# Kernel tuning notes

Measured on AMD Instinct MI355X. Metric: run time of the kernel, lower is better.

The kernel has to match this reference:

```python
import jax, jax.numpy as jnp
import numpy as np

B, S, DMODEL = 1, 2048, 4096
H, HKV, DH = 32, 8, 128
LTAB, RBKT = 20, 128
NEG = -1e9


def rotate_half(x):
    x1, x2 = x[..., : x.shape[-1] // 2], x[..., x.shape[-1] // 2:]
    return jnp.concatenate((-x2, x1), axis=-1)


def setup_inputs() -> dict:
    key = jax.random.key(0)
    ks = jax.random.split(key, 12)
    inp = {
        "hidden_states": jax.random.normal(ks[0], (B, S, DMODEL), jnp.float32),
        "cos": jax.random.uniform(ks[1], (B, S, DH), jnp.float32),
        "sin": jax.random.uniform(ks[2], (B, S, DH), jnp.float32),
        "q_probs": jax.random.uniform(ks[3], (B, H, LTAB, RBKT), jnp.float32),
        "v_norm": jax.random.uniform(ks[4], (B, H, S), jnp.float32),
        "allowed": jnp.ones((B, H, S), dtype=bool),
        "k_hard": jax.random.randint(ks[5], (B, H, LTAB, S), 0, RBKT, jnp.int32),
        "Wq": jax.random.normal(ks[6], (DMODEL, H * DH), jnp.float32) * 0.02,
        "Wk": jax.random.normal(ks[7], (DMODEL, HKV * DH), jnp.float32) * 0.02,
        "Wv": jax.random.normal(ks[8], (DMODEL, HKV * DH), jnp.float32) * 0.02,
        "Wo": jax.random.normal(ks[9], (H * DH, DMODEL), jnp.float32) * 0.02,
        "sink": 4,
        "window": 128,
        "M": 256,
    }
    return inp


def _sparse_key_mask(q_probs, v_norm, allowed, k_hard, sink, window, M):
    """Faithful jax version of build_sparse_list_decode, returned as a boolean
    allowed-key mask [B, H, T] (equivalent to scattering sparse_list)."""
    Bm, Hm, _, T = k_hard.shape
    # soft-hash collision score: sum over tables of q bucket prob at key's bucket,
    # weighted by value-norm history, restricted to allowed keys.
    coll = jnp.take_along_axis(q_probs, k_hard.astype(jnp.int32), axis=-1).sum(axis=2)  # [B,H,T]
    scores = jnp.where(allowed, coll * v_norm, -jnp.inf)
    M_eff = min(M, T)
    mask = jnp.zeros((Bm, Hm, T), dtype=bool)
    if M_eff > 0:
        heavy_idx = jax.lax.top_k(scores, M_eff)[1]  # [B,H,M]
        b_ix = jnp.arange(Bm)[:, None, None]
        h_ix = jnp.arange(Hm)[None, :, None]
        mask = mask.at[b_ix, h_ix, heavy_idx].set(True)
    sink = max(0, min(sink, T))
    window = max(0, min(window, T))
    if sink > 0:
        mask = mask.at[:, :, :sink].set(True)
    if window > 0:
        win_start = max(T - window, sink)
        if win_start < T:
            mask = mask.at[:, :, win_start:].set(True)
    if sink == 0 and window == 0:
        mask = mask.at[:, :, T - 1].set(True)
    return mask & allowed


def reference(hidden_states, cos, sin, q_probs, v_norm, allowed, k_hard,
              Wq, Wk, Wv, Wo, sink, window, M):
    Bx, Sx, _ = hidden_states.shape
    scaling = DH ** -0.5
    q = (hidden_states @ Wq).reshape(Bx, Sx, H, DH).transpose(0, 2, 1, 3)   # [B,H,S,Dh]
    k = (hidden_states @ Wk).reshape(Bx, Sx, HKV, DH).transpose(0, 2, 1, 3)  # [B,Hkv,S,Dh]
    v = (hidden_states @ Wv).reshape(Bx, Sx, HKV, DH).transpose(0, 2, 1, 3)
    # RoPE (unsqueeze_dim=1)
    c, s = cos[:, None, :, :], sin[:, None, :, :]
    q = q * c + rotate_half(q) * s
    k = k * c + rotate_half(k) * s
    # repeat_kv for GQA
    n_rep = H // HKV
    k = jnp.repeat(k, n_rep, axis=1)
    v = jnp.repeat(v, n_rep, axis=1)
    # sparse heavy-hitter + sink + window key mask (no_grad in the original)
    key_mask = _sparse_key_mask(q_probs, v_norm, allowed, k_hard, sink, window, M)  # [B,H,S]
    causal = jnp.tril(jnp.ones((Sx, Sx), dtype=bool))
    allow = causal[None, None] & key_mask[:, :, None, :]  # [B,H,S,S]
    scores = jnp.einsum('bhqd,bhkd->bhqk', q, k) * scaling
    attn = jax.nn.softmax(jnp.where(allow, scores, NEG), axis=-1)
    out = jnp.einsum('bhqk,bhkd->bhqd', attn, v)
    out = out.transpose(0, 2, 1, 3).reshape(Bx, Sx, H * DH)
    return out @ Wo
```

## Files before the change

kernel.cpp:

```cpp
#include <hip/hip_runtime.h>
#include <hip/hip_bf16.h>
#include <cstdint>
#include <cstddef>

namespace {

constexpr int S_LEN = 2048;
constexpr int DM    = 4096;
constexpr int NH    = 32;
constexpr int NKV   = 8;
constexpr int DH    = 128;
constexpr int LTAB  = 20;
constexpr int RBKT  = 128;
constexpr int NQKV  = NH * DH + 2 * NKV * DH;
constexpr int KOFF  = NH * DH;
constexpr int VOFF  = NH * DH + NKV * DH;

typedef short s16x8 __attribute__((ext_vector_type(8)));
typedef float f32x4 __attribute__((ext_vector_type(4)));
typedef unsigned long long u64;
struct u64x2 { u64 x, y; };

__device__ inline short bf16s(float f) {
  __hip_bfloat16 b = __float2bfloat16(f);
  return (short)*reinterpret_cast<unsigned short*>(&b);
}
__device__ inline float s2f(short s) {
  unsigned short u = (unsigned short)s;
  return __bfloat162float(*reinterpret_cast<__hip_bfloat16*>(&u));
}

__global__ __launch_bounds__(256) void cvt_f32_bf16(const float* __restrict__ in,
                                                    __hip_bfloat16* __restrict__ out,
                                                    int n4) {
  int i = blockIdx.x * blockDim.x + threadIdx.x;
  if (i >= n4) return;
  float4 v = reinterpret_cast<const float4*>(in)[i];
  ushort4 o;
  o.x = (unsigned short)bf16s(v.x);
  o.y = (unsigned short)bf16s(v.y);
  o.z = (unsigned short)bf16s(v.z);
  o.w = (unsigned short)bf16s(v.w);
  reinterpret_cast<ushort4*>(out)[i] = o;
}

__global__ __launch_bounds__(256) void transpose_cvt64(const float* __restrict__ W,
                                                       __hip_bfloat16* __restrict__ Wt,
                                                       int K, int N) {
  __shared__ float tile[64][65];
  const int kb = blockIdx.y * 64, nb = blockIdx.x * 64;
  const int tid = threadIdx.x;
  const int r0 = tid >> 4, c4 = (tid & 15) * 4;
#pragma unroll
  for (int it = 0; it < 4; ++it) {
    const int r = r0 + it * 16;
    float4 v = *reinterpret_cast<const float4*>(&W[(size_t)(kb + r) * N + nb + c4]);
    tile[r][c4] = v.x;
    tile[r][c4 + 1] = v.y;
    tile[r][c4 + 2] = v.z;
    tile[r][c4 + 3] = v.w;
  }
  __syncthreads();
  const int n0 = tid >> 4, k4 = (tid & 15) * 4;
#pragma unroll
  for (int it = 0; it < 4; ++it) {
    const int n = n0 + it * 16;
    ushort4 o;
    o.x = (unsigned short)bf16s(tile[k4][n]);
    o.y = (unsigned short)bf16s(tile[k4 + 1][n]);
    o.z = (unsigned short)bf16s(tile[k4 + 2][n]);
    o.w = (unsigned short)bf16s(tile[k4 + 3][n]);
    *reinterpret_cast<ushort4*>(&Wt[(size_t)(nb + n) * K + kb + k4]) = o;
  }
}

template <bool OUT_F32>
__global__ __launch_bounds__(256) void gemm_bt(const __hip_bfloat16* __restrict__ A,
                                               const __hip_bfloat16* __restrict__ Bt,
                                               void* __restrict__ Cout,
                                               int N, int K) {
  __shared__ __hip_bfloat16 As[128 * 64];
  __shared__ __hip_bfloat16 Bs[128 * 64];
  const int tid = threadIdx.x;
  const int wid = tid >> 6;
  const int lane = tid & 63;
  const int bm = blockIdx.y, bn = blockIdx.x;
  const int wr = wid >> 1, wc = wid & 1;
  f32x4 acc[4][4] = {};
  const __hip_bfloat16* Abase = A + (size_t)bm * 128 * K;
  const __hip_bfloat16* Bbase = Bt + (size_t)bn * 128 * K;
  for (int kt = 0; kt < K; kt += 64) {
    __syncthreads();
#pragma unroll
    for (int j = 0; j < 4; ++j) {
      const int pb = j * 4096 + wid * 1024;
      const int p = pb + lane * 16;
      const int row = p >> 7;
      const int slot = ((p >> 4) & 7) ^ (row & 7);
      const int goff = row * K + kt + slot * 8;
      __builtin_amdgcn_global_load_lds(
          (const __attribute__((address_space(1))) void*)(Abase + goff),
          (__attribute__((address_space(3))) void*)(As + (pb >> 1)), 16, 0, 0);
      __builtin_amdgcn_global_load_lds(
          (const __attribute__((address_space(1))) void*)(Bbase + goff),
          (__attribute__((address_space(3))) void*)(Bs + (pb >> 1)), 16, 0, 0);
    }
    __syncthreads();
#pragma unroll
    for (int kk = 0; kk < 2; ++kk) {
      s16x8 af[4], bf[4];
#pragma unroll
      for (int i = 0; i < 4; ++i) {
        const int ra = wr * 64 + i * 16 + (lane & 15);
        const int sa = (kk * 4 + (lane >> 4)) ^ (ra & 7);
        af[i] = *reinterpret_cast<const s16x8*>(As + ra * 64 + sa * 8);
        const int rb = wc * 64 + i * 16 + (lane & 15);
        const int sb = (kk * 4 + (lane >> 4)) ^ (rb & 7);
        bf[i] = *reinterpret_cast<const s16x8*>(Bs + rb * 64 + sb * 8);
      }
#pragma unroll
      for (int i = 0; i < 4; ++i)
#pragma unroll
        for (int jn = 0; jn < 4; ++jn)
          acc[i][jn] = __builtin_amdgcn_mfma_f32_16x16x32_bf16(af[i], bf[jn], acc[i][jn], 0, 0, 0);
    }
  }
  const int rg = (lane >> 4) * 4;
  const int cg = lane & 15;
#pragma unroll
  for (int i = 0; i < 4; ++i)
#pragma unroll
    for (int jn = 0; jn < 4; ++jn)
#pragma unroll
      for (int r = 0; r < 4; ++r) {
        const int rr = bm * 128 + wr * 64 + i * 16 + rg + r;
        const int cc = bn * 128 + wc * 64 + jn * 16 + cg;
        if (OUT_F32)
          reinterpret_cast<float*>(Cout)[(size_t)rr * N + cc] = acc[i][jn][r];
        else
          reinterpret_cast<__hip_bfloat16*>(Cout)[(size_t)rr * N + cc] =
              __float2bfloat16(acc[i][jn][r]);
      }
}

__global__ __launch_bounds__(256) void rope_kernel(const __hip_bfloat16* __restrict__ QKV,
                                                   const float* __restrict__ cosb,
                                                   const float* __restrict__ sinb,
                                                   __hip_bfloat16* __restrict__ Qro,
                                                   __hip_bfloat16* __restrict__ Kro) {
  const int s = blockIdx.x;
  const int tid = threadIdx.x;
  const float* cs = cosb + s * DH;
  const float* sn = sinb + s * DH;
  const __hip_bfloat16* row = QKV + (size_t)s * NQKV;
  for (int ch = tid; ch < 512 + 128; ch += 256) {
    const bool isQ = ch < 512;
    const int idx8 = (isQ ? ch : ch - 512) * 8;
    const int d8 = idx8 & (DH - 1);
    const int hb = idx8 - d8;
    const __hip_bfloat16* src = isQ ? row : row + KOFF;
    s16x8 v = *reinterpret_cast<const s16x8*>(src + idx8);
    s16x8 p = *reinterpret_cast<const s16x8*>(src + hb + (d8 ^ 64));
    const float sgn = (d8 < 64) ? -1.f : 1.f;
    s16x8 outv;
#pragma unroll
    for (int j = 0; j < 8; ++j) {
      const float r = s2f(v[j]) * cs[d8 + j] + sgn * s2f(p[j]) * sn[d8 + j];
      outv[j] = bf16s(r);
    }
    if (isQ)
      *reinterpret_cast<s16x8*>(Qro + (size_t)s * (NH * DH) + idx8) = outv;
    else
      *reinterpret_cast<s16x8*>(Kro + (size_t)s * (NKV * DH) + idx8) = outv;
  }
}

__global__ __launch_bounds__(1024) void select_kernel(const float* __restrict__ q_probs,
                                                      const float* __restrict__ v_norm,
                                                      const int* __restrict__ allowed,
                                                      const int* __restrict__ k_hard,
                                                      const int* __restrict__ sinkp,
                                                      const int* __restrict__ winp,
                                                      const int* __restrict__ Mp,
                                                      int* __restrict__ sel_idx,
                                                      int* __restrict__ sel_cnt) {
  const int h = blockIdx.x;
  const int tid = threadIdx.x;
  const int lane = tid & 63;
  const int wid = tid >> 6;
  __shared__ u64 keys[S_LEN];
  __shared__ int waveTot[16];
  const int t0 = tid * 2;
  float c0 = 0.f, c1 = 0.f;
#pragma unroll
  for (int l = 0; l < LTAB; ++l) {
    const int2 kh = *reinterpret_cast<const int2*>(&k_hard[(size_t)(h * LTAB + l) * S_LEN + t0]);
    c0 += q_probs[(h * LTAB + l) * RBKT + kh.x];
    c1 += q_probs[(h * LTAB + l) * RBKT + kh.y];
  }
  const int2 al = *reinterpret_cast<const int2*>(&allowed[h * S_LEN + t0]);
  const float2 vn = *reinterpret_cast<const float2*>(&v_norm[h * S_LEN + t0]);
  const float s0 = al.x ? c0 * vn.x : -INFINITY;
  const float s1 = al.y ? c1 * vn.y : -INFINITY;
  auto mkkey = [](float s, int t) -> u64 {
    unsigned m = __float_as_uint(s);
    m = (m & 0x80000000u) ? ~m : (m | 0x80000000u);
    return ((u64)m << 11) | (u64)(S_LEN - 1 - t);
  };
  const u64 k0 = mkkey(s0, t0);
  const u64 k1 = mkkey(s1, t0 + 1);
  keys[t0] = k0;
  keys[t0 + 1] = k1;
  __syncthreads();
  int r0 = 0, r1 = 0;
#pragma unroll 8
  for (int u = 0; u < S_LEN; u += 2) {
    const u64x2 kv = *reinterpret_cast<const u64x2*>(&keys[u]);
    r0 += (kv.x > k0) + (kv.y > k0);
    r1 += (kv.x > k1) + (kv.y > k1);
  }
  const int Mv = min(Mp[0], S_LEN);
  int sv = sinkp[0];
  sv = sv < 0 ? 0 : (sv > S_LEN ? S_LEN : sv);
  int wv = winp[0];
  wv = wv < 0 ? 0 : (wv > S_LEN ? S_LEN : wv);
  int wstart = S_LEN - wv;
  if (wstart < sv) wstart = sv;
  bool sel0 = r0 < Mv, sel1 = r1 < Mv;
  if (t0 < sv) sel0 = true;
  if (t0 + 1 < sv) sel1 = true;
  if (wv > 0) {
    if (t0 >= wstart) sel0 = true;
    if (t0 + 1 >= wstart) sel1 = true;
  }
  if (sv == 0 && wv == 0) {
    if (t0 == S_LEN - 1) sel0 = true;
    if (t0 + 1 == S_LEN - 1) sel1 = true;
  }
  sel0 = sel0 && (al.x != 0);
  sel1 = sel1 && (al.y != 0);
  const int cnt = (sel0 ? 1 : 0) + (sel1 ? 1 : 0);
  int inc = cnt;
#pragma unroll
  for (int off = 1; off < 64; off <<= 1) {
    int n = __shfl_up(inc, off);
    if (lane >= off) inc += n;
  }
  if (lane == 63) waveTot[wid] = inc;
  __syncthreads();
  int wbase = 0;
  for (int w = 0; w < wid; ++w) wbase += waveTot[w];
  int pos = wbase + inc - cnt;
  if (tid == 0) {
    int tot = 0;
#pragma unroll
    for (int w = 0; w < 16; ++w) tot += waveTot[w];
    sel_cnt[h] = tot;
  }
  if (sel0) sel_idx[h * S_LEN + pos++] = t0;
  if (sel1) sel_idx[h * S_LEN + pos] = t0 + 1;
}

__global__ __launch_bounds__(256) void attn_kernel(const __hip_bfloat16* __restrict__ Qro,
                                                   const __hip_bfloat16* __restrict__ Kro,
                                                   const __hip_bfloat16* __restrict__ Vpk,
                                                   const int* __restrict__ sel_idx,
                                                   const int* __restrict__ sel_cnt,
                                                   __hip_bfloat16* __restrict__ ctx) {
  constexpr int BKV = 32;
  const int h = blockIdx.y;
  const int q0 = blockIdx.x * 64;
  const int tid = threadIdx.x, wid = tid >> 6, lane = tid & 63;
  const int kv = h >> 2;
  __shared__ __hip_bfloat16 Ks[BKV][DH + 8];
  __shared__ __hip_bfloat16 Vt[DH][BKV + 8];
  __shared__ __hip_bfloat16 Ps[4][16][BKV + 8];
  __shared__ int tIdx[BKV];
  const int qbase = q0 + wid * 16;
  const float scaling = 0.08838834764831845f;
  s16x8 qf[4];
  {
    const __hip_bfloat16* qp =
        Qro + (size_t)(qbase + (lane & 15)) * (NH * DH) + h * DH + (lane >> 4) * 8;
#pragma unroll
    for (int kt = 0; kt < 4; ++kt) {
      s16x8 q = *reinterpret_cast<const s16x8*>(qp + kt * 32);
#pragma unroll
      for (int j = 0; j < 8; ++j) q[j] = bf16s(s2f(q[j]) * scaling);
      qf[kt] = q;
    }
  }
  float mr[4], lr[4];
#pragma unroll
  for (int r = 0; r < 4; ++r) {
    mr[r] = -3.0e38f;
    lr[r] = 0.f;
  }
  f32x4 o[8] = {};
  const int cnt = sel_cnt[h];
  const int qmax = q0 + 63;
  for (int j0 = 0; j0 < cnt; j0 += BKV) {
    if (sel_idx[h * S_LEN + j0] > qmax) break;
    const int nk = min(BKV, cnt - j0);
    __syncthreads();
    if (tid < BKV) tIdx[tid] = (tid < nk) ? sel_idx[h * S_LEN + j0 + tid] : 0x7fffffff;
#pragma unroll
    for (int c = 0; c < 2; ++c) {
      const int ch = tid + c * 256;
      const int row = ch >> 4, c8 = ch & 15;
      if (row < nk) {
        const int t = sel_idx[h * S_LEN + j0 + row];
        *reinterpret_cast<s16x8*>(&Ks[row][c8 * 8]) = *reinterpret_cast<const s16x8*>(
            Kro + (size_t)t * (NKV * DH) + kv * DH + c8 * 8);
      }
    }
    {
      const int j = tid >> 3;
      const int dp = (tid & 7) * 16;
      if (j < nk) {
        const int t = sel_idx[h * S_LEN + j0 + j];
        const __hip_bfloat16* vp = Vpk + (size_t)t * NQKV + kv * DH + dp;
        s16x8 a = *reinterpret_cast<const s16x8*>(vp);
        s16x8 b = *reinterpret_cast<const s16x8*>(vp + 8);
#pragma unroll
        for (int i = 0; i < 8; ++i) reinterpret_cast<short&>(Vt[dp + i][j]) = a[i];
#pragma unroll
        for (int i = 0; i < 8; ++i) reinterpret_cast<short&>(Vt[dp + 8 + i][j]) = b[i];
      } else {
#pragma unroll
        for (int i = 0; i < 16; ++i) reinterpret_cast<short&>(Vt[dp + i][j]) = 0;
      }
    }
    __syncthreads();
    f32x4 s0 = {0.f, 0.f, 0.f, 0.f}, s1 = {0.f, 0.f, 0.f, 0.f};
#pragma unroll
    for (int kt = 0; kt < 4; ++kt) {
      s16x8 k0 = *reinterpret_cast<const s16x8*>(&Ks[lane & 15][kt * 32 + (lane >> 4) * 8]);
      s16x8 k1 = *reinterpret_cast<const s16x8*>(&Ks[16 + (lane & 15)][kt * 32 + (lane >> 4) * 8]);
      s0 = __builtin_amdgcn_mfma_f32_16x16x32_bf16(qf[kt], k0, s0, 0, 0, 0);
      s1 = __builtin_amdgcn_mfma_f32_16x16x32_bf16(qf[kt], k1, s1, 0, 0, 0);
    }
    const int t0 = tIdx[lane & 15];
    const int t1 = tIdx[16 + (lane & 15)];
    float v0[4], v1[4], mx[4];
    bool need = false;
#pragma unroll
    for (int r = 0; r < 4; ++r) {
      const int qs = qbase + ((lane >> 4) << 2) + r;
      v0[r] = (t0 <= qs) ? s0[r] : -1.0e9f;
      v1[r] = (t1 <= qs) ? s1[r] : -1.0e9f;
      float m = fmaxf(v0[r], v1[r]);
#pragma unroll
      for (int off = 1; off < 16; off <<= 1) m = fmaxf(m, __shfl_xor(m, off));
      mx[r] = m;
      need = need || (m > mr[r] + 8.f);
    }
    if (__any(need)) {
#pragma unroll
      for (int r = 0; r < 4; ++r) {
        const float mn = fmaxf(mr[r], mx[r]);
        const float scl = __expf(mr[r] - mn);
        lr[r] *= scl;
#pragma unroll
        for (int nt = 0; nt < 8; ++nt) o[nt][r] *= scl;
        mr[r] = mn;
      }
    }
#pragma unroll
    for (int r = 0; r < 4; ++r) {
      const float p0 = __expf(v0[r] - mr[r]);
      const float p1 = __expf(v1[r] - mr[r]);
      float ps = p0 + p1;
#pragma unroll
      for (int off = 1; off < 16; off <<= 1) ps += __shfl_xor(ps, off);
      lr[r] += ps;
      Ps[wid][((lane >> 4) << 2) + r][lane & 15] = __float2bfloat16(p0);
      Ps[wid][((lane >> 4) << 2) + r][16 + (lane & 15)] = __float2bfloat16(p1);
    }
    const s16x8 pf = *reinterpret_cast<const s16x8*>(&Ps[wid][lane & 15][(lane >> 4) * 8]);
#pragma unroll
    for (int nt = 0; nt < 8; ++nt) {
      const s16x8 vf =
          *reinterpret_cast<const s16x8*>(&Vt[nt * 16 + (lane & 15)][(lane >> 4) * 8]);
      o[nt] = __builtin_amdgcn_mfma_f32_16x16x32_bf16(pf, vf, o[nt], 0, 0, 0);
    }
  }
#pragma unroll
  for (int nt = 0; nt < 8; ++nt)
#pragma unroll
    for (int r = 0; r < 4; ++r) {
      const int qs = qbase + ((lane >> 4) << 2) + r;
      const int d = nt * 16 + (lane & 15);
      ctx[(size_t)qs * (NH * DH) + h * DH + d] = __float2bfloat16(o[nt][r] / lr[r]);
    }
}

}

extern "C" void kernel_launch(void* const* d_in, const int* in_sizes, int n_in,
                              void* d_out, int out_size, void* d_ws, size_t ws_size,
                              hipStream_t stream) {
  const float* hidden = (const float*)d_in[0];
  const float* cosb = (const float*)d_in[1];
  const float* sinb = (const float*)d_in[2];
  const float* q_probs = (const float*)d_in[3];
  const float* v_norm = (const float*)d_in[4];
  const int* allowed = (const int*)d_in[5];
  const int* k_hard = (const int*)d_in[6];
  const float* Wq = (const float*)d_in[7];
  const float* Wk = (const float*)d_in[8];
  const float* Wv = (const float*)d_in[9];
  const float* Wo = (const float*)d_in[10];
  const int* sinkp = (const int*)d_in[11];
  const int* winp = (const int*)d_in[12];
  const int* Mp = (const int*)d_in[13];

  char* ws = (char*)d_ws;
  size_t off = 0;
  auto alloc = [&](size_t bytes) -> char* {
    char* p = ws + off;
    off += (bytes + 255) & ~(size_t)255;
    return p;
  };
  __hip_bfloat16* hbf = (__hip_bfloat16*)alloc((size_t)S_LEN * DM * 2);
  __hip_bfloat16* WqkvT = (__hip_bfloat16*)alloc((size_t)NQKV * DM * 2);
  __hip_bfloat16* WoT = (__hip_bfloat16*)alloc((size_t)DM * DM * 2);
  __hip_bfloat16* QKV = (__hip_bfloat16*)alloc((size_t)S_LEN * NQKV * 2);
  __hip_bfloat16* Qro = (__hip_bfloat16*)alloc((size_t)S_LEN * NH * DH * 2);
  __hip_bfloat16* Kro = (__hip_bfloat16*)alloc((size_t)S_LEN * NKV * DH * 2);
  __hip_bfloat16* ctx = (__hip_bfloat16*)alloc((size_t)S_LEN * NH * DH * 2);
  int* sel_idx = (int*)alloc((size_t)NH * S_LEN * 4);
  int* sel_cnt = (int*)alloc((size_t)NH * 4);
  if (off > ws_size) return;

  {
    const int n4 = S_LEN * DM / 4;
    cvt_f32_bf16<<<(n4 + 255) / 256, 256, 0, stream>>>(hidden, hbf, n4);
  }
  transpose_cvt64<<<dim3(DM / 64, DM / 64), 256, 0, stream>>>(Wq, WqkvT, DM, DM);
  transpose_cvt64<<<dim3((NKV * DH) / 64, DM / 64), 256, 0, stream>>>(
      Wk, WqkvT + (size_t)KOFF * DM, DM, NKV * DH);
  transpose_cvt64<<<dim3((NKV * DH) / 64, DM / 64), 256, 0, stream>>>(
      Wv, WqkvT + (size_t)VOFF * DM, DM, NKV * DH);
  transpose_cvt64<<<dim3(DM / 64, DM / 64), 256, 0, stream>>>(Wo, WoT, DM, DM);

  gemm_bt<false><<<dim3(NQKV / 128, S_LEN / 128), 256, 0, stream>>>(
      hbf, WqkvT, (void*)QKV, NQKV, DM);

  rope_kernel<<<S_LEN, 256, 0, stream>>>(QKV, cosb, sinb, Qro, Kro);

  select_kernel<<<NH, 1024, 0, stream>>>(q_probs, v_norm, allowed, k_hard, sinkp, winp, Mp,
                                         sel_idx, sel_cnt);

  attn_kernel<<<dim3(S_LEN / 64, NH), 256, 0, stream>>>(Qro, Kro, QKV + VOFF, sel_idx,
                                                        sel_cnt, ctx);

  gemm_bt<true><<<dim3(DM / 128, S_LEN / 128), 256, 0, stream>>>(ctx, WoT, d_out, DM, DM);
}
```

Measured before the change: 431.2 us.

## Swizzle GEMM block order and compute softmax row sums via MFMA

The GEMM remaps workgroup IDs so that consecutive blocks are interleaved across eight groups, aiming for better cache locality across XCDs. In the sparse attention kernel, the per-row max shuffle reduction now runs only when a rescale is triggered, using a per-lane threshold test. The row-sum shuffle reduction is replaced by an MFMA of the bf16 probabilities against a ones vector. The row sum therefore accumulates the bf16-rounded probabilities, which keeps it consistent with the PV product but changes numerics slightly.

```diff
diff --git a/kernel.cpp b/kernel.cpp
--- a/kernel.cpp
+++ b/kernel.cpp
@@ -84,7 +84,20 @@
   const int tid = threadIdx.x;
   const int wid = tid >> 6;
   const int lane = tid & 63;
-  const int bm = blockIdx.y, bn = blockIdx.x;
+  int bm, bn;
+  {
+    const int nwg = gridDim.x * gridDim.y;
+    const int orig = blockIdx.y * gridDim.x + blockIdx.x;
+    if ((nwg & 7) == 0) {
+      const int cpx = nwg >> 3;
+      const int id2 = (orig & 7) * cpx + (orig >> 3);
+      bm = id2 / gridDim.x;
+      bn = id2 % gridDim.x;
+    } else {
+      bm = blockIdx.y;
+      bn = blockIdx.x;
+    }
+  }
   const int wr = wid >> 1, wc = wid & 1;
   f32x4 acc[4][4] = {};
   const __hip_bfloat16* Abase = A + (size_t)bm * 128 * K;
@@ -290,6 +303,9 @@
       qf[kt] = q;
     }
   }
+  s16x8 ones;
+#pragma unroll
+  for (int j = 0; j < 8; ++j) ones[j] = (short)0x3F80;
   float mr[4], lr[4];
 #pragma unroll
   for (int r = 0; r < 4; ++r) {
@@ -342,23 +358,22 @@
     }
     const int t0 = tIdx[lane & 15];
     const int t1 = tIdx[16 + (lane & 15)];
-    float v0[4], v1[4], mx[4];
+    float v0[4], v1[4];
     bool need = false;
 #pragma unroll
     for (int r = 0; r < 4; ++r) {
       const int qs = qbase + ((lane >> 4) << 2) + r;
       v0[r] = (t0 <= qs) ? s0[r] : -1.0e9f;
       v1[r] = (t1 <= qs) ? s1[r] : -1.0e9f;
-      float m = fmaxf(v0[r], v1[r]);
-#pragma unroll
-      for (int off = 1; off < 16; off <<= 1) m = fmaxf(m, __shfl_xor(m, off));
-      mx[r] = m;
-      need = need || (m > mr[r] + 8.f);
+      need = need || (fmaxf(v0[r], v1[r]) > mr[r] + 8.f);
     }
     if (__any(need)) {
 #pragma unroll
       for (int r = 0; r < 4; ++r) {
-        const float mn = fmaxf(mr[r], mx[r]);
+        float m = fmaxf(v0[r], v1[r]);
+#pragma unroll
+        for (int off = 1; off < 16; off <<= 1) m = fmaxf(m, __shfl_xor(m, off));
+        const float mn = fmaxf(mr[r], m);
         const float scl = __expf(mr[r] - mn);
         lr[r] *= scl;
 #pragma unroll
@@ -370,14 +385,16 @@
     for (int r = 0; r < 4; ++r) {
       const float p0 = __expf(v0[r] - mr[r]);
       const float p1 = __expf(v1[r] - mr[r]);
-      float ps = p0 + p1;
-#pragma unroll
-      for (int off = 1; off < 16; off <<= 1) ps += __shfl_xor(ps, off);
-      lr[r] += ps;
       Ps[wid][((lane >> 4) << 2) + r][lane & 15] = __float2bfloat16(p0);
       Ps[wid][((lane >> 4) << 2) + r][16 + (lane & 15)] = __float2bfloat16(p1);
     }
     const s16x8 pf = *reinterpret_cast<const s16x8*>(&Ps[wid][lane & 15][(lane >> 4) * 8]);
+    {
+      f32x4 zero = {0.f, 0.f, 0.f, 0.f};
+      f32x4 psum = __builtin_amdgcn_mfma_f32_16x16x32_bf16(pf, ones, zero, 0, 0, 0);
+#pragma unroll
+      for (int r = 0; r < 4; ++r) lr[r] += psum[r];
+    }
 #pragma unroll
     for (int nt = 0; nt < 8; ++nt) {
       const s16x8 vf =
```

After: 422.7 us. -2.0%, faster.
